# Performance work log

Measured on AMD Instinct MI355X. Metric: run time of the kernel, lower is better.

The kernel has to match this reference:

```python
import jax, jax.numpy as jnp
import numpy as np

PATCH = 14
MERGE = 2
HIDDEN = 1024
# (H, W) in pixels; all multiples of PATCH with even patch grids (divisible by MERGE)
IMAGE_SIZES = np.array([[1540, 1540], [1120, 1540], [1540, 896], [784, 1260],
                        [1512, 1512], [1540, 1120], [896, 896], [1260, 1540]], dtype=np.int64)


def setup_inputs() -> dict:
    key = jax.random.key(0)
    k1, k2 = jax.random.split(key)
    sizes_p = IMAGE_SIZES // PATCH
    total_tokens = int((sizes_p[:, 0] * sizes_p[:, 1]).sum())  # 67440
    image_features = jax.random.normal(k1, (total_tokens, HIDDEN), dtype=jnp.float32)
    # nn.Linear(hidden*merge**2 -> hidden, bias=False): weight shape [out, in] = [1024, 4096]
    merging_weight = jax.random.normal(k2, (HIDDEN, HIDDEN * MERGE * MERGE), dtype=jnp.float32) * 0.02
    image_sizes = jnp.asarray(IMAGE_SIZES)
    return {"image_features": image_features, "merging_weight": merging_weight, "image_sizes": image_sizes}


def _merge_patches(feats, sizes_np):
    """Per-image unfold(kernel=MERGE, stride=MERGE) over the [hp, wp] patch grid.
    torch unfold orders the flattened channel dim as d*m*m + ki*m + kj (channel-major),
    blocks in row-major (i, j) order -> reshape/transpose below reproduces it exactly."""
    m = MERGE
    D = feats.shape[-1]
    out, off = [], 0
    for h, w in sizes_np:  # small fixed set of images (static shapes)
        hp, wp = int(h) // PATCH, int(w) // PATCH
        n = hp * wp
        g = jax.lax.dynamic_slice_in_dim(feats, off, n, axis=0)
        g = g.reshape(hp // m, m, wp // m, m, D)          # [i, ki, j, kj, d]
        g = g.transpose(0, 2, 4, 1, 3).reshape(-1, D * m * m)  # [i*j, d*ki*kj]
        out.append(g)
        off += n
    return jnp.concatenate(out, axis=0)  # [total_tokens / m^2, D*m^2]


def reference(image_features, merging_weight, image_sizes):
    sizes_np = np.asarray(jax.device_get(image_sizes))  # static metadata
    merged = _merge_patches(image_features, sizes_np)
    return merged @ merging_weight.T  # [total/4, HIDDEN]
```

## Files before the change

### kernel.cpp

```cpp
#include <hip/hip_runtime.h>
#include <hip/hip_bf16.h>

#define MTOK  16860
#define MPAD  16896
#define NOUT  1024
#define KDIM  4096

__device__ __constant__ int c_mend[8] = {3025,5225,6985,8245,11161,13361,14385,16860};
__device__ __constant__ int c_moff[8] = {0,3025,5225,6985,8245,11161,13361,14385};
__device__ __constant__ int c_foff[8] = {0,12100,20900,27940,32980,44644,53444,57540};
__device__ __constant__ int c_wp[8]   = {110,110,64,90,108,80,64,110};

typedef __attribute__((ext_vector_type(8))) short          bf16x8;
typedef __attribute__((ext_vector_type(8))) unsigned short u16x8;
typedef __attribute__((ext_vector_type(4))) float          f32x4;

__device__ __forceinline__ unsigned short f2bf(float f) {
    unsigned int u = __float_as_uint(f);
    u += 0x7FFFu + ((u >> 16) & 1u);
    return (unsigned short)(u >> 16);
}

__device__ __forceinline__ void async_copy16(const void* g, void* l) {
    __builtin_amdgcn_global_load_lds(
        (const __attribute__((address_space(1))) void*)g,
        (__attribute__((address_space(3))) void*)l, 16, 0, 0);
}

__global__ __launch_bounds__(256) void merge_cast(const float* __restrict__ feats,
                                                  unsigned short* __restrict__ merged) {
    const int d = threadIdx.x * 4;
#pragma unroll
    for (int it = 0; it < 4; ++it) {
        int t = blockIdx.x * 4 + it;
        if (t >= MTOK) return;
        int im = 0;
        while (t >= c_mend[im]) im++;
        int r   = t - c_moff[im];
        int wp  = c_wp[im];
        int wp2 = wp >> 1;
        int i = r / wp2, j = r - i * wp2;
        const float* p00 = feats + (size_t)(c_foff[im] + (2*i)*wp + 2*j) * 1024;
        const float* p01 = p00 + 1024;
        const float* p10 = p00 + (size_t)wp * 1024;
        const float* p11 = p10 + 1024;
        float4 a = *(const float4*)(p00 + d);
        float4 b = *(const float4*)(p01 + d);
        float4 c = *(const float4*)(p10 + d);
        float4 e = *(const float4*)(p11 + d);
        u16x8 lo, hi;
        lo[0]=f2bf(a.x); lo[1]=f2bf(b.x); lo[2]=f2bf(c.x); lo[3]=f2bf(e.x);
        lo[4]=f2bf(a.y); lo[5]=f2bf(b.y); lo[6]=f2bf(c.y); lo[7]=f2bf(e.y);
        hi[0]=f2bf(a.z); hi[1]=f2bf(b.z); hi[2]=f2bf(c.z); hi[3]=f2bf(e.z);
        hi[4]=f2bf(a.w); hi[5]=f2bf(b.w); hi[6]=f2bf(c.w); hi[7]=f2bf(e.w);
        unsigned short* o = merged + (size_t)t * 4096 + d * 4;
        *(u16x8*)(o)     = lo;
        *(u16x8*)(o + 8) = hi;
    }
}

__global__ __launch_bounds__(256) void cast_w(const float* __restrict__ W,
                                              unsigned short* __restrict__ Wb) {
    size_t g = (size_t)(blockIdx.x * 256 + threadIdx.x) * 4;
    float4 v = *(const float4*)(W + g);
    *(ushort4*)(Wb + g) = make_ushort4(f2bf(v.x), f2bf(v.y), f2bf(v.z), f2bf(v.w));
}

#define BM 128
#define BN 128
#define BK 32
__global__ __launch_bounds__(256) void gemm_bt(const unsigned short* __restrict__ A,
                                               const unsigned short* __restrict__ B,
                                               float* __restrict__ C) {
    __shared__ unsigned short lA[BM * BK];
    __shared__ unsigned short lB[BN * BK];

    const int bn = blockIdx.x, bm = blockIdx.y;
    const int tid  = threadIdx.x;
    const int wave = tid >> 6, lane = tid & 63;
    const int wm = (wave >> 1) * 64, wn = (wave & 1) * 64;

    const int lrow = lane >> 2;
    const int lcol = (lane & 3) * 8;

    const unsigned short* Abase = A + (size_t)bm * 128 * KDIM;
    const unsigned short* Bbase = B + (size_t)bn * 128 * KDIM;

    f32x4 acc[4][4];
#pragma unroll
    for (int i = 0; i < 4; ++i)
#pragma unroll
        for (int j = 0; j < 4; ++j) acc[i][j] = (f32x4){0.f, 0.f, 0.f, 0.f};

    const int mrow = lane & 15;
    const int kq   = (lane >> 4) * 8;

    for (int k0 = 0; k0 < KDIM; k0 += BK) {
#pragma unroll
        for (int r = 0; r < 2; ++r) {
            int chunk = wave + r * 4;
            int row   = chunk * 16 + lrow;
            async_copy16(Abase + (size_t)row * KDIM + k0 + lcol, &lA[chunk * 512 + lane * 8]);
            async_copy16(Bbase + (size_t)row * KDIM + k0 + lcol, &lB[chunk * 512 + lane * 8]);
        }
        __syncthreads();

        bf16x8 af[4], bfr[4];
#pragma unroll
        for (int i = 0; i < 4; ++i) {
            af[i]  = *(const bf16x8*)&lA[(wm + i * 16 + mrow) * BK + kq];
            bfr[i] = *(const bf16x8*)&lB[(wn + i * 16 + mrow) * BK + kq];
        }
#pragma unroll
        for (int i = 0; i < 4; ++i)
#pragma unroll
            for (int j = 0; j < 4; ++j)
                acc[i][j] = __builtin_amdgcn_mfma_f32_16x16x32_bf16(af[i], bfr[j], acc[i][j], 0, 0, 0);
        __syncthreads();
    }

    const int col   = lane & 15;
    const int rquad = (lane >> 4) * 4;
#pragma unroll
    for (int i = 0; i < 4; ++i) {
        int gm0 = bm * 128 + wm + i * 16 + rquad;
#pragma unroll
        for (int j = 0; j < 4; ++j) {
            int gn = bn * 128 + wn + j * 16 + col;
#pragma unroll
            for (int rg = 0; rg < 4; ++rg) {
                int gm = gm0 + rg;
                if (gm < MTOK) C[(size_t)gm * NOUT + gn] = acc[i][j][rg];
            }
        }
    }
}

__global__ __launch_bounds__(256) void naive_fb(const float* __restrict__ feats,
                                                const float* __restrict__ W,
                                                float* __restrict__ out) {
    int t = blockIdx.x;
    int o = blockIdx.y * 256 + threadIdx.x;
    int im = 0;
    while (t >= c_mend[im]) im++;
    int r = t - c_moff[im];
    int wp = c_wp[im], wp2 = wp >> 1;
    int i = r / wp2, j = r - i * wp2;
    const float* f00 = feats + (size_t)(c_foff[im] + (2*i)*wp + 2*j) * 1024;
    const float* f10 = f00 + (size_t)wp * 1024;
    const float* w = W + (size_t)o * 4096;
    float s = 0.f;
    for (int d = 0; d < 1024; ++d)
        s += f00[d] * w[d*4] + f00[d+1024] * w[d*4+1] + f10[d] * w[d*4+2] + f10[d+1024] * w[d*4+3];
    out[(size_t)t * 1024 + o] = s;
}

extern "C" void kernel_launch(void* const* d_in, const int* in_sizes, int n_in,
                              void* d_out, int out_size, void* d_ws, size_t ws_size,
                              hipStream_t stream) {
    const float* feats = (const float*)d_in[0];
    const float* W     = (const float*)d_in[1];
    float* out         = (float*)d_out;

    const size_t need = ((size_t)MPAD + 1024) * KDIM * sizeof(unsigned short);
    if (ws_size >= need) {
        unsigned short* merged = (unsigned short*)d_ws;
        unsigned short* Wb     = merged + (size_t)MPAD * KDIM;
        merge_cast<<<dim3((MTOK + 3) / 4), 256, 0, stream>>>(feats, merged);
        cast_w<<<dim3((NOUT * KDIM / 4) / 256), 256, 0, stream>>>(W, Wb);
        gemm_bt<<<dim3(NOUT / BN, MPAD / BM), 256, 0, stream>>>(merged, Wb, out);
    } else {
        naive_fb<<<dim3(MTOK, 4), 256, 0, stream>>>(feats, W, out);
    }
}
```

Measured before the change: 711.7 us.

## Fuse patch-merge and bf16 cast into GEMM A-tile loading

Removes the separate merge_cast kernel and its bf16 staging buffer. The GEMM now reads fp32 features directly from the four 2x2 patch neighbours, converts them to bf16 in registers, and writes them into the LDS A tile, prefetching the next k-step into registers. This saves the write and reread of a roughly 138MB intermediate. In exchange, each A row is re-read in fp32 by all 8 N-blocks, so A traffic grows, and A loads become synchronous register loads instead of async LDS copies.

Result: slower. 1.306 ms (+83.5%).

```diff
diff --git a/kernel.cpp b/kernel.cpp
--- a/kernel.cpp
+++ b/kernel.cpp
@@ -27,38 +27,6 @@
         (__attribute__((address_space(3))) void*)l, 16, 0, 0);
 }
 
-__global__ __launch_bounds__(256) void merge_cast(const float* __restrict__ feats,
-                                                  unsigned short* __restrict__ merged) {
-    const int d = threadIdx.x * 4;
-#pragma unroll
-    for (int it = 0; it < 4; ++it) {
-        int t = blockIdx.x * 4 + it;
-        if (t >= MTOK) return;
-        int im = 0;
-        while (t >= c_mend[im]) im++;
-        int r   = t - c_moff[im];
-        int wp  = c_wp[im];
-        int wp2 = wp >> 1;
-        int i = r / wp2, j = r - i * wp2;
-        const float* p00 = feats + (size_t)(c_foff[im] + (2*i)*wp + 2*j) * 1024;
-        const float* p01 = p00 + 1024;
-        const float* p10 = p00 + (size_t)wp * 1024;
-        const float* p11 = p10 + 1024;
-        float4 a = *(const float4*)(p00 + d);
-        float4 b = *(const float4*)(p01 + d);
-        float4 c = *(const float4*)(p10 + d);
-        float4 e = *(const float4*)(p11 + d);
-        u16x8 lo, hi;
-        lo[0]=f2bf(a.x); lo[1]=f2bf(b.x); lo[2]=f2bf(c.x); lo[3]=f2bf(e.x);
-        lo[4]=f2bf(a.y); lo[5]=f2bf(b.y); lo[6]=f2bf(c.y); lo[7]=f2bf(e.y);
-        hi[0]=f2bf(a.z); hi[1]=f2bf(b.z); hi[2]=f2bf(c.z); hi[3]=f2bf(e.z);
-        hi[4]=f2bf(a.w); hi[5]=f2bf(b.w); hi[6]=f2bf(c.w); hi[7]=f2bf(e.w);
-        unsigned short* o = merged + (size_t)t * 4096 + d * 4;
-        *(u16x8*)(o)     = lo;
-        *(u16x8*)(o + 8) = hi;
-    }
-}
-
 __global__ __launch_bounds__(256) void cast_w(const float* __restrict__ W,
                                               unsigned short* __restrict__ Wb) {
     size_t g = (size_t)(blockIdx.x * 256 + threadIdx.x) * 4;
@@ -69,9 +37,9 @@
 #define BM 128
 #define BN 128
 #define BK 32
-__global__ __launch_bounds__(256) void gemm_bt(const unsigned short* __restrict__ A,
-                                               const unsigned short* __restrict__ B,
-                                               float* __restrict__ C) {
+__global__ __launch_bounds__(256) void gemm_fused(const float* __restrict__ feats,
+                                                  const unsigned short* __restrict__ B,
+                                                  float* __restrict__ C) {
     __shared__ unsigned short lA[BM * BK];
     __shared__ unsigned short lB[BN * BK];
 
@@ -83,54 +51,93 @@
     const int lrow = lane >> 2;
     const int lcol = (lane & 3) * 8;
 
-    const unsigned short* Abase = A + (size_t)bm * 128 * KDIM;
-    const unsigned short* Bbase = B + (size_t)bn * 128 * KDIM;
+    const int r    = tid >> 1;
+    const int half = tid & 1;
+    const int trow = bm * BM + r;
+    const bool valid = (trow < MTOK);
+    {
+    }
+    int tt = valid ? trow : 0;
+    int im = 0;
+    while (tt >= c_mend[im]) im++;
+    int rr  = tt - c_moff[im];
+    int wp  = c_wp[im];
+    int wp2 = wp >> 1;
+    int i = rr / wp2, j = rr - i * wp2;
+    const float* p00 = feats + (size_t)(c_foff[im] + (2*i)*wp + 2*j) * 1024 + half * 4;
+    const float* p01 = p00 + 1024;
+    const float* p10 = p00 + (size_t)wp * 1024;
+    const float* p11 = p10 + 1024;
+
+    const unsigned short* Bbase = B + (size_t)bn * BN * KDIM;
 
     f32x4 acc[4][4];
 #pragma unroll
-    for (int i = 0; i < 4; ++i)
+    for (int a = 0; a < 4; ++a)
 #pragma unroll
-        for (int j = 0; j < 4; ++j) acc[i][j] = (f32x4){0.f, 0.f, 0.f, 0.f};
+        for (int b = 0; b < 4; ++b) acc[a][b] = (f32x4){0.f, 0.f, 0.f, 0.f};
 
     const int mrow = lane & 15;
     const int kq   = (lane >> 4) * 8;
 
+    float4 va = *(const float4*)(p00);
+    float4 vb = *(const float4*)(p01);
+    float4 vc = *(const float4*)(p10);
+    float4 vd = *(const float4*)(p11);
+
     for (int k0 = 0; k0 < KDIM; k0 += BK) {
+        u16x8 lo, hi;
+        lo[0]=f2bf(va.x); lo[1]=f2bf(vb.x); lo[2]=f2bf(vc.x); lo[3]=f2bf(vd.x);
+        lo[4]=f2bf(va.y); lo[5]=f2bf(vb.y); lo[6]=f2bf(vc.y); lo[7]=f2bf(vd.y);
+        hi[0]=f2bf(va.z); hi[1]=f2bf(vb.z); hi[2]=f2bf(vc.z); hi[3]=f2bf(vd.z);
+        hi[4]=f2bf(va.w); hi[5]=f2bf(vb.w); hi[6]=f2bf(vc.w); hi[7]=f2bf(vd.w);
+        if (!valid) { lo = (u16x8)0; hi = (u16x8)0; }
+        unsigned short* dst = &lA[r * BK + half * 16];
+        *(u16x8*)(dst)     = lo;
+        *(u16x8*)(dst + 8) = hi;
+
 #pragma unroll
-        for (int r = 0; r < 2; ++r) {
-            int chunk = wave + r * 4;
+        for (int r2 = 0; r2 < 2; ++r2) {
+            int chunk = wave * 2 + r2;
             int row   = chunk * 16 + lrow;
-            async_copy16(Abase + (size_t)row * KDIM + k0 + lcol, &lA[chunk * 512 + lane * 8]);
             async_copy16(Bbase + (size_t)row * KDIM + k0 + lcol, &lB[chunk * 512 + lane * 8]);
         }
         __syncthreads();
 
+        int doffn = ((k0 + BK) & (KDIM - 1)) >> 2;
+        float4 na = *(const float4*)(p00 + doffn);
+        float4 nb = *(const float4*)(p01 + doffn);
+        float4 nc = *(const float4*)(p10 + doffn);
+        float4 nd = *(const float4*)(p11 + doffn);
+
         bf16x8 af[4], bfr[4];
 #pragma unroll
-        for (int i = 0; i < 4; ++i) {
-            af[i]  = *(const bf16x8*)&lA[(wm + i * 16 + mrow) * BK + kq];
-            bfr[i] = *(const bf16x8*)&lB[(wn + i * 16 + mrow) * BK + kq];
+        for (int a = 0; a < 4; ++a) {
+            af[a]  = *(const bf16x8*)&lA[(wm + a * 16 + mrow) * BK + kq];
+            bfr[a] = *(const bf16x8*)&lB[(wn + a * 16 + mrow) * BK + kq];
         }
 #pragma unroll
-        for (int i = 0; i < 4; ++i)
+        for (int a = 0; a < 4; ++a)
 #pragma unroll
-            for (int j = 0; j < 4; ++j)
-                acc[i][j] = __builtin_amdgcn_mfma_f32_16x16x32_bf16(af[i], bfr[j], acc[i][j], 0, 0, 0);
+            for (int b = 0; b < 4; ++b)
+                acc[a][b] = __builtin_amdgcn_mfma_f32_16x16x32_bf16(af[a], bfr[b], acc[a][b], 0, 0, 0);
         __syncthreads();
+
+        va = na; vb = nb; vc = nc; vd = nd;
     }
 
     const int col   = lane & 15;
     const int rquad = (lane >> 4) * 4;
 #pragma unroll
-    for (int i = 0; i < 4; ++i) {
-        int gm0 = bm * 128 + wm + i * 16 + rquad;
+    for (int a = 0; a < 4; ++a) {
+        int gm0 = bm * BM + wm + a * 16 + rquad;
 #pragma unroll
-        for (int j = 0; j < 4; ++j) {
-            int gn = bn * 128 + wn + j * 16 + col;
+        for (int b = 0; b < 4; ++b) {
+            int gn = bn * BN + wn + b * 16 + col;
 #pragma unroll
             for (int rg = 0; rg < 4; ++rg) {
                 int gm = gm0 + rg;
-                if (gm < MTOK) C[(size_t)gm * NOUT + gn] = acc[i][j][rg];
+                if (gm < MTOK) C[(size_t)gm * NOUT + gn] = acc[a][b][rg];
             }
         }
     }
@@ -162,13 +169,11 @@
     const float* W     = (const float*)d_in[1];
     float* out         = (float*)d_out;
 
-    const size_t need = ((size_t)MPAD + 1024) * KDIM * sizeof(unsigned short);
+    const size_t need = (size_t)NOUT * KDIM * sizeof(unsigned short);
     if (ws_size >= need) {
-        unsigned short* merged = (unsigned short*)d_ws;
-        unsigned short* Wb     = merged + (size_t)MPAD * KDIM;
-        merge_cast<<<dim3((MTOK + 3) / 4), 256, 0, stream>>>(feats, merged);
+        unsigned short* Wb = (unsigned short*)d_ws;
         cast_w<<<dim3((NOUT * KDIM / 4) / 256), 256, 0, stream>>>(W, Wb);
-        gemm_bt<<<dim3(NOUT / BN, MPAD / BM), 256, 0, stream>>>(merged, Wb, out);
+        gemm_fused<<<dim3(NOUT / BN, MPAD / BM), 256, 0, stream>>>(feats, Wb, out);
     } else {
         naive_fb<<<dim3(MTOK, 4), 256, 0, stream>>>(feats, W, out);
     }
```
